# Optimization experiments

Measured on AMD Instinct MI355X. Metric: run time of the kernel, lower is better.

The kernel has to match this reference:

```python
import jax, jax.numpy as jnp
import numpy as np

VOCAB = 33
D = 256
B = 64
L = 4096


def setup_inputs() -> dict:
    key = jax.random.key(0)
    ks = jax.random.split(key, 7)
    X = jax.random.randint(ks[0], (B, L), 0, VOCAB, dtype=jnp.int64)
    valid_lens = jax.random.randint(ks[1], (B,), 0, L, dtype=jnp.int64)
    emb = jax.random.normal(ks[2], (VOCAB, D), dtype=jnp.float32)
    W1 = jax.random.normal(ks[3], (D, D), dtype=jnp.float32) * (1.0 / np.sqrt(D))
    b1 = jnp.zeros((D,), dtype=jnp.float32)
    W2 = jax.random.normal(ks[4], (D, D), dtype=jnp.float32) * (1.0 / np.sqrt(D))
    b2 = jnp.zeros((D,), dtype=jnp.float32)
    return {"X": X, "valid_lens": valid_lens, "emb": emb, "W1": W1, "b1": b1, "W2": W2, "b2": b2}


def reference(X, valid_lens, emb, W1, b1, W2, b2):
    # Embedding gather: [B, L, D]
    e = emb[X]
    # Length mask (on-device, no python loop): positions >= valid_len zeroed
    mask = (jnp.arange(L)[None, :] < valid_lens[:, None]).astype(e.dtype)  # [B, L]
    # Masked sum-pool over sequence -> [B, D]
    pooled = jnp.einsum("bld,bl->bd", e, mask)
    # Two-layer MLP with ReLU (dropout is identity in eval)
    h = jax.nn.relu(pooled @ W1 + b1)
    out = jax.nn.relu(h @ W2 + b2)
    return out
```

## Files before the change

kernel.cpp:

```cpp
#include <hip/hip_runtime.h>

#define B_SZ  64
#define L_SZ  4096
#define VOCAB 33
#define D_SZ  256
#define NT    512
#define NW    8
#define C     64

__global__ __launch_bounds__(NT) void prot_fused(
    const int* __restrict__ X,
    const int* __restrict__ valid_lens,
    const float* __restrict__ emb,
    const float* __restrict__ W1,
    const float* __restrict__ b1,
    const float* __restrict__ W2,
    const float* __restrict__ b2,
    float* __restrict__ out)
{
    __shared__ int    s_cnt[NW][VOCAB];
    __shared__ float4 s_part[NW][C];
    __shared__ float  s_vec[D_SZ];

    const int bid = blockIdx.x;
    const int b   = bid >> 2;
    const int cg  = bid & 3;
    const int t   = threadIdx.x;
    const int g   = t >> 6;
    const int c   = t & 63;

    const float4* emb4 = reinterpret_cast<const float4*>(emb);
    const float4* W14  = reinterpret_cast<const float4*>(W1);

    float w2[32];
    #pragma unroll
    for (int q = 0; q < 32; ++q)
        w2[q] = W2[(g * 32 + q) * D_SZ + cg * 64 + c];

    float4 e4[4];
    #pragma unroll
    for (int j = 0; j < 4; ++j)
        e4[j] = emb4[(g * 4 + j) * C + c];
    float4 e32 = make_float4(0.f, 0.f, 0.f, 0.f);
    if (g == 0) e32 = emb4[32 * C + c];

    float4 bias1 = make_float4(0.f, 0.f, 0.f, 0.f);
    if (t < C) bias1 = reinterpret_cast<const float4*>(b1)[t];
    const float bias2 = (t < 64) ? b2[cg * 64 + t] : 0.f;

    const int   vl    = valid_lens[b];
    const int4* xrow4 = reinterpret_cast<const int4*>(X + (size_t)b * L_SZ);
    const int4  t0    = xrow4[t];
    const int4  t1    = xrow4[t + NT];

    if (t < NW * VOCAB) ((int*)s_cnt)[t] = 0;
    __syncthreads();

    const int l0 = t * 4;
    const int l1 = (t + NT) * 4;
    if (l0 + 0 < vl) atomicAdd(&s_cnt[g][t0.x], 1);
    if (l0 + 1 < vl) atomicAdd(&s_cnt[g][t0.y], 1);
    if (l0 + 2 < vl) atomicAdd(&s_cnt[g][t0.z], 1);
    if (l0 + 3 < vl) atomicAdd(&s_cnt[g][t0.w], 1);
    if (l1 + 0 < vl) atomicAdd(&s_cnt[g][t1.x], 1);
    if (l1 + 1 < vl) atomicAdd(&s_cnt[g][t1.y], 1);
    if (l1 + 2 < vl) atomicAdd(&s_cnt[g][t1.z], 1);
    if (l1 + 3 < vl) atomicAdd(&s_cnt[g][t1.w], 1);
    __syncthreads();

    float cf[4];
    #pragma unroll
    for (int j = 0; j < 4; ++j) {
        int s = 0;
        #pragma unroll
        for (int w = 0; w < NW; ++w) s += s_cnt[w][g * 4 + j];
        cf[j] = (float)s;
    }
    float c32 = 0.f;
    if (g == 0) {
        int s = 0;
        #pragma unroll
        for (int w = 0; w < NW; ++w) s += s_cnt[w][32];
        c32 = (float)s;
    }

    float4 p = make_float4(0.f, 0.f, 0.f, 0.f);
    #pragma unroll
    for (int j = 0; j < 4; ++j) {
        p.x = fmaf(cf[j], e4[j].x, p.x);
        p.y = fmaf(cf[j], e4[j].y, p.y);
        p.z = fmaf(cf[j], e4[j].z, p.z);
        p.w = fmaf(cf[j], e4[j].w, p.w);
    }
    p.x = fmaf(c32, e32.x, p.x);
    p.y = fmaf(c32, e32.y, p.y);
    p.z = fmaf(c32, e32.z, p.z);
    p.w = fmaf(c32, e32.w, p.w);
    s_part[g][c] = p;
    __syncthreads();

    if (t < C) {
        float4 s = s_part[0][t];
        #pragma unroll
        for (int g2 = 1; g2 < NW; ++g2) {
            float4 q = s_part[g2][t];
            s.x += q.x; s.y += q.y; s.z += q.z; s.w += q.w;
        }
        reinterpret_cast<float4*>(s_vec)[t] = s;
    }
    __syncthreads();

    float4 acc = make_float4(0.f, 0.f, 0.f, 0.f);
    #pragma unroll
    for (int j = 0; j < 32; ++j) {
        const int   k  = g * 32 + j;
        const float sv = s_vec[k];
        const float4 w = W14[k * C + c];
        acc.x = fmaf(sv, w.x, acc.x);
        acc.y = fmaf(sv, w.y, acc.y);
        acc.z = fmaf(sv, w.z, acc.z);
        acc.w = fmaf(sv, w.w, acc.w);
    }
    s_part[g][c] = acc;
    __syncthreads();

    if (t < C) {
        float4 h = bias1;
        #pragma unroll
        for (int g2 = 0; g2 < NW; ++g2) {
            float4 q = s_part[g2][t];
            h.x += q.x; h.y += q.y; h.z += q.z; h.w += q.w;
        }
        h.x = fmaxf(h.x, 0.f); h.y = fmaxf(h.y, 0.f);
        h.z = fmaxf(h.z, 0.f); h.w = fmaxf(h.w, 0.f);
        reinterpret_cast<float4*>(s_vec)[t] = h;
    }
    __syncthreads();

    float acc2 = 0.f;
    #pragma unroll
    for (int q = 0; q < 32; ++q)
        acc2 = fmaf(s_vec[g * 32 + q], w2[q], acc2);
    ((float*)s_part)[g * 64 + c] = acc2;
    __syncthreads();

    if (t < 64) {
        float o = bias2;
        #pragma unroll
        for (int q = 0; q < NW; ++q) o += ((float*)s_part)[q * 64 + t];
        out[(size_t)b * D_SZ + cg * 64 + t] = fmaxf(o, 0.f);
    }
}

extern "C" void kernel_launch(void* const* d_in, const int* in_sizes, int n_in,
                              void* d_out, int out_size, void* d_ws, size_t ws_size,
                              hipStream_t stream) {
    const int*   X          = (const int*)d_in[0];
    const int*   valid_lens = (const int*)d_in[1];
    const float* emb        = (const float*)d_in[2];
    const float* W1         = (const float*)d_in[3];
    const float* b1         = (const float*)d_in[4];
    const float* W2         = (const float*)d_in[5];
    const float* b2         = (const float*)d_in[6];
    float* out = (float*)d_out;

    prot_fused<<<256, NT, 0, stream>>>(X, valid_lens, emb, W1, b1, W2, b2, out);
}
```

Measured before the change: 10.96 us.

## Prefetch W1 into registers and use LDS-only barriers to overlap global loads

Issues the X token loads first, then preloads each thread's 32 float4 W1 slice into registers right after the histogram atomics, before the first barrier. This lets the W1 fetch overlap the histogram and pooling phases instead of waiting on global memory inside the first GEMV loop. `__syncthreads` is replaced by a custom barrier that waits only on LDS counters, not on vector memory, so outstanding global loads stay in flight across barriers. The separate barrier after zeroing the counts is removed: each wavefront now zeroes its own count row, which relies on in-wave ordering. The cost is much higher register pressure, roughly 128 extra VGPRs per thread.

```diff
diff --git a/kernel.cpp b/kernel.cpp
--- a/kernel.cpp
+++ b/kernel.cpp
@@ -7,6 +7,13 @@
 #define NT    512
 #define NW    8
 #define C     64
+
+#define LBAR()                                            \
+    do {                                                  \
+        asm volatile("s_waitcnt lgkmcnt(0)" ::: "memory");\
+        __builtin_amdgcn_s_barrier();                     \
+        __builtin_amdgcn_sched_barrier(0);                \
+    } while (0)
 
 __global__ __launch_bounds__(NT) void prot_fused(
     const int* __restrict__ X,
@@ -32,6 +39,11 @@
     const float4* emb4 = reinterpret_cast<const float4*>(emb);
     const float4* W14  = reinterpret_cast<const float4*>(W1);
 
+    const int   vl    = valid_lens[b];
+    const int4* xrow4 = reinterpret_cast<const int4*>(X + (size_t)b * L_SZ);
+    const int4  t0    = xrow4[t];
+    const int4  t1    = xrow4[t + NT];
+
     float w2[32];
     #pragma unroll
     for (int q = 0; q < 32; ++q)
@@ -48,13 +60,7 @@
     if (t < C) bias1 = reinterpret_cast<const float4*>(b1)[t];
     const float bias2 = (t < 64) ? b2[cg * 64 + t] : 0.f;
 
-    const int   vl    = valid_lens[b];
-    const int4* xrow4 = reinterpret_cast<const int4*>(X + (size_t)b * L_SZ);
-    const int4  t0    = xrow4[t];
-    const int4  t1    = xrow4[t + NT];
-
-    if (t < NW * VOCAB) ((int*)s_cnt)[t] = 0;
-    __syncthreads();
+    if (c < VOCAB) s_cnt[g][c] = 0;
 
     const int l0 = t * 4;
     const int l1 = (t + NT) * 4;
@@ -66,7 +72,13 @@
     if (l1 + 1 < vl) atomicAdd(&s_cnt[g][t1.y], 1);
     if (l1 + 2 < vl) atomicAdd(&s_cnt[g][t1.z], 1);
     if (l1 + 3 < vl) atomicAdd(&s_cnt[g][t1.w], 1);
-    __syncthreads();
+
+    float4 w1[32];
+    #pragma unroll
+    for (int j = 0; j < 32; ++j)
+        w1[j] = W14[(g * 32 + j) * C + c];
+
+    LBAR();
 
     float cf[4];
     #pragma unroll
@@ -97,7 +109,7 @@
     p.z = fmaf(c32, e32.z, p.z);
     p.w = fmaf(c32, e32.w, p.w);
     s_part[g][c] = p;
-    __syncthreads();
+    LBAR();
 
     if (t < C) {
         float4 s = s_part[0][t];
@@ -108,21 +120,19 @@
         }
         reinterpret_cast<float4*>(s_vec)[t] = s;
     }
-    __syncthreads();
+    LBAR();
 
     float4 acc = make_float4(0.f, 0.f, 0.f, 0.f);
     #pragma unroll
     for (int j = 0; j < 32; ++j) {
-        const int   k  = g * 32 + j;
-        const float sv = s_vec[k];
-        const float4 w = W14[k * C + c];
-        acc.x = fmaf(sv, w.x, acc.x);
-        acc.y = fmaf(sv, w.y, acc.y);
-        acc.z = fmaf(sv, w.z, acc.z);
-        acc.w = fmaf(sv, w.w, acc.w);
+        const float sv = s_vec[g * 32 + j];
+        acc.x = fmaf(sv, w1[j].x, acc.x);
+        acc.y = fmaf(sv, w1[j].y, acc.y);
+        acc.z = fmaf(sv, w1[j].z, acc.z);
+        acc.w = fmaf(sv, w1[j].w, acc.w);
     }
     s_part[g][c] = acc;
-    __syncthreads();
+    LBAR();
 
     if (t < C) {
         float4 h = bias1;
@@ -135,14 +145,14 @@
         h.z = fmaxf(h.z, 0.f); h.w = fmaxf(h.w, 0.f);
         reinterpret_cast<float4*>(s_vec)[t] = h;
     }
-    __syncthreads();
+    LBAR();
 
     float acc2 = 0.f;
     #pragma unroll
     for (int q = 0; q < 32; ++q)
         acc2 = fmaf(s_vec[g * 32 + q], w2[q], acc2);
     ((float*)s_part)[g * 64 + c] = acc2;
-    __syncthreads();
+    LBAR();
 
     if (t < 64) {
         float o = bias2;
```

New measurement: 10.32 us. -5.8%, faster.
